# Optimization experiments

Hardware: AMD Instinct MI355X
Metric: run time of the kernel (lower is better)

## Reference

```python
import jax, jax.numpy as jnp
import numpy as np

B, L, D_MODEL = 2, 2048, 1024
HEADS, DH, K = 8, 128, 64  # d_head = d_model // heads, kernel_width window
DILATIONS = np.array([1, 1, 2, 2, 4, 4, 8, 8], dtype=np.int32)  # per-head dilation


def setup_inputs() -> dict:
    key = jax.random.key(0)
    ks = jax.random.split(key, 8)
    s_in = 1.0 / np.sqrt(D_MODEL)       # kaiming-uniform-ish fan_in bound
    s_c = 1.0 / np.sqrt(HEADS * DH)
    return {
        "query": jax.random.normal(ks[0], (B, L, D_MODEL), dtype=jnp.float32),
        "key": jax.random.normal(ks[1], (B, L, D_MODEL), dtype=jnp.float32),
        "value": jax.random.normal(ks[2], (B, L, D_MODEL), dtype=jnp.float32),
        "Wq": jax.random.uniform(ks[3], (HEADS, DH, D_MODEL), minval=-s_in, maxval=s_in),
        "bq": jnp.zeros((HEADS, DH), dtype=jnp.float32),
        "Wk": jax.random.uniform(ks[4], (HEADS, DH, D_MODEL), minval=-s_in, maxval=s_in),
        "bk": jnp.zeros((HEADS, DH), dtype=jnp.float32),
        "Wv": jax.random.uniform(ks[5], (HEADS, DH, D_MODEL), minval=-s_in, maxval=s_in),
        "bv": jnp.zeros((HEADS, DH), dtype=jnp.float32),
        "Wc": jax.random.uniform(ks[6], (D_MODEL, HEADS * DH), minval=-s_c, maxval=s_c),
        "bc": jnp.zeros((D_MODEL,), dtype=jnp.float32),
    }


def reference(query, key, value, Wq, bq, Wk, bk, Wv, bv, Wc, bc):
    Lq = query.shape[-2]
    # per-head linear projections: [B,L,D] x [H,DH,D] -> [B,H,L,DH]
    q = jnp.einsum('bld,hed->bhle', query, Wq) + bq[:, None, :]
    k = jnp.einsum('bld,hed->bhle', key, Wk) + bk[:, None, :]
    v = jnp.einsum('bld,hed->bhle', value, Wv) + bv[:, None, :]

    # dilated, centered local windows (per-head dilation)
    offsets = jnp.arange(K) - (K - 1) // 2                     # [K]
    dil = jnp.asarray(DILATIONS)                               # [H]
    idx = (jnp.arange(Lq)[None, :, None]
           + offsets[None, None, :] * dil[:, None, None])      # [H, L, K]
    valid = (idx >= 0) & (idx < Lq)
    idxc = jnp.clip(idx, 0, Lq - 1)

    # gather per-head windows: x [B,H,L,DH], idx [H,L,K] -> [B,H,L,K,DH]
    gather = jax.vmap(lambda xh, ih: xh[:, ih], in_axes=(1, 0), out_axes=1)
    k_win = gather(k, idxc)
    v_win = gather(v, idxc)

    # banded attention (original applies no 1/sqrt(d) scaling)
    scores = jnp.einsum('bhld,bhlkd->bhlk', q, k_win)
    scores = jnp.where(valid[None], scores, jnp.asarray(-1e9, scores.dtype))
    attn = jax.nn.softmax(scores, axis=-1)
    out = jnp.einsum('bhlk,bhlkd->bhld', attn, v_win)

    # merge heads and collapse back to d_model
    out = out.transpose(0, 2, 1, 3).reshape(out.shape[0], Lq, HEADS * DH)
    return out @ Wc.T + bc
```

## Files before the change

### kernel.cpp

```cpp
#include <hip/hip_runtime.h>
#include <hip/hip_bf16.h>
#include <stdint.h>

#define NB 2
#define LQ 2048
#define DMODEL 1024
#define NH 8
#define DH 128
#define KWIN 64

typedef __attribute__((ext_vector_type(8))) short short8;
typedef __attribute__((ext_vector_type(4))) float f32x4;

#define AS1 __attribute__((address_space(1)))
#define AS3 __attribute__((address_space(3)))

__device__ __forceinline__ ushort f2bf(float f) {
  uint u = __float_as_uint(f);
  return (ushort)((u + 0x7fffu + ((u >> 16) & 1u)) >> 16);
}

__global__ void cvt_all(const float4* __restrict__ q, const float4* __restrict__ k,
                        const float4* __restrict__ v, const float4* __restrict__ wq,
                        const float4* __restrict__ wk, const float4* __restrict__ wv,
                        const float4* __restrict__ wc, ushort4* __restrict__ dst) {
  const int n4in = (NB * LQ * DMODEL) / 4;
  const int n4w = (NH * DH * DMODEL) / 4;
  const int total = 3 * n4in + 4 * n4w;
  const int stride = gridDim.x * blockDim.x;
  for (int i = blockIdx.x * blockDim.x + threadIdx.x; i < total; i += stride) {
    const float4* src;
    int off;
    if (i < 3 * n4in) {
      const int r = i >> 20;
      off = i & (n4in - 1);
      src = (r == 0) ? q : ((r == 1) ? k : v);
    } else {
      const int j = i - 3 * n4in;
      const int r = j >> 18;
      off = j & (n4w - 1);
      src = (r == 0) ? wq : ((r == 1) ? wk : ((r == 2) ? wv : wc));
    }
    float4 x = src[off];
    dst[i] = make_ushort4(f2bf(x.x), f2bf(x.y), f2bf(x.z), f2bf(x.w));
  }
}

__global__ __launch_bounds__(512, 2) void gemm256_8p(
    const ushort* __restrict__ A0p, const ushort* __restrict__ B0p,
    const float* __restrict__ c0, ushort* __restrict__ D0,
    const ushort* __restrict__ A1p, const ushort* __restrict__ B1p,
    const float* __restrict__ c1, ushort* __restrict__ D1,
    const ushort* __restrict__ A2p, const ushort* __restrict__ B2p,
    const float* __restrict__ c2, ushort* __restrict__ D2,
    int M, int N, int Kd) {
  const int gx = gridDim.x, gy = gridDim.y;
  const int nblk = gx * gy * gridDim.z;
  const int fid = (blockIdx.z * gy + blockIdx.y) * gx + blockIdx.x;
  const int nid = (fid & 7) * (nblk >> 3) + (fid >> 3);
  const int z = nid / (gx * gy);
  const int rem = nid % (gx * gy);
  const int m0 = (rem / gx) * 256;
  const int n0 = (rem % gx) * 256;

  const ushort* A = (z == 0) ? A0p : ((z == 1) ? A1p : A2p);
  const ushort* Bt = (z == 0) ? B0p : ((z == 1) ? B1p : B2p);
  const float* bias = (z == 0) ? c0 : ((z == 1) ? c1 : c2);
  ushort* Cv = (z == 0) ? D0 : ((z == 1) ? D1 : D2);

  __shared__ ushort LDS[2][32768];

  const int tid = threadIdx.x;
  const int wave = tid >> 6, lane = tid & 63;
  const int wm = wave >> 2, wn = wave & 3;
  const int lrow = lane & 15, kgrp = lane >> 4;

  int offA[2][2], offB[2][2];
#pragma unroll
  for (int u = 0; u < 2; ++u)
#pragma unroll
    for (int j = 0; j < 2; ++j) {
      const int idx = j * 512 + tid;
      const int s = idx >> 3, c = idx & 7;
      const int cs = c ^ (s & 7);
      const int rA = ((s >> 6) << 7) | (u << 6) | (s & 63);
      const int rB = ((s >> 5) << 6) | (u << 5) | (s & 31);
      offA[u][j] = (m0 + rA) * Kd + cs * 8;
      offB[u][j] = (n0 + rB) * Kd + cs * 8;
    }

  auto STAGEA = [&](int bufb, int u, int T) {
    ushort* dst = &LDS[bufb][u * 8192];
#pragma unroll
    for (int j = 0; j < 2; ++j)
      __builtin_amdgcn_global_load_lds((const AS1 void*)(A + offA[u][j] + T * 64),
                                       (AS3 void*)(dst + (j * 512 + tid) * 8), 16, 0, 0);
  };
  auto STAGEB = [&](int bufb, int u, int T) {
    ushort* dst = &LDS[bufb][16384 + u * 8192];
#pragma unroll
    for (int j = 0; j < 2; ++j)
      __builtin_amdgcn_global_load_lds((const AS1 void*)(Bt + offB[u][j] + T * 64),
                                       (AS3 void*)(dst + (j * 512 + tid) * 8), 16, 0, 0);
  };

  const int sAb = (wm * 64 + lrow) * 64;
  const int sBb = (wn * 32 + lrow) * 64;
  int xk[2];
#pragma unroll
  for (int ks = 0; ks < 2; ++ks) xk[ks] = ((ks * 4 + kgrp) ^ (lrow & 7)) * 8;

  short8 af[4][2], bf[2][2][2];
  f32x4 acc[8][4] = {};

  auto RDA = [&](int bufb, int mh) {
#pragma unroll
    for (int mi = 0; mi < 4; ++mi)
#pragma unroll
      for (int ks = 0; ks < 2; ++ks)
        af[mi][ks] = *(const short8*)(&LDS[bufb][mh * 8192 + sAb + mi * 1024 + xk[ks]]);
  };
  auto RDB = [&](int bufb, int nh) {
#pragma unroll
    for (int ni = 0; ni < 2; ++ni)
#pragma unroll
      for (int ks = 0; ks < 2; ++ks)
        bf[nh][ni][ks] =
            *(const short8*)(&LDS[bufb][16384 + nh * 8192 + sBb + ni * 1024 + xk[ks]]);
  };
  auto MM = [&](int mh, int nh) {
    __builtin_amdgcn_s_setprio(1);
#pragma unroll
    for (int mi = 0; mi < 4; ++mi)
#pragma unroll
      for (int ni = 0; ni < 2; ++ni)
#pragma unroll
        for (int ks = 0; ks < 2; ++ks)
          acc[mh * 4 + mi][nh * 2 + ni] = __builtin_amdgcn_mfma_f32_16x16x32_bf16(
              af[mi][ks], bf[nh][ni][ks], acc[mh * 4 + mi][nh * 2 + ni], 0, 0, 0);
    __builtin_amdgcn_s_setprio(0);
  };

#define LGKM0()                                        \
  asm volatile("s_waitcnt lgkmcnt(0)" ::: "memory");   \
  __builtin_amdgcn_sched_barrier(0)
#define BAR() __builtin_amdgcn_s_barrier()

  const int NKT = Kd >> 6;
  const int NIT = NKT >> 1;

  STAGEA(0, 0, 0); STAGEB(0, 0, 0); STAGEA(0, 1, 0); STAGEB(0, 1, 0);
  STAGEA(1, 0, 1); STAGEB(1, 0, 1);
  asm volatile("s_waitcnt vmcnt(4)" ::: "memory");
  __builtin_amdgcn_sched_barrier(0);
  BAR();

  for (int i = 0; i < NIT; ++i) {
    const int ta = 2 * i, tb = ta + 1;
    const bool sA = (ta + 2) < NKT, sB = (tb + 2) < NKT;
    RDA(0, 0); RDB(0, 0);
    STAGEA(1, 1, tb);
    BAR(); LGKM0(); MM(0, 0); BAR();
    RDB(0, 1);
    STAGEB(1, 1, tb);
    BAR(); LGKM0(); MM(0, 1); BAR();
    RDA(0, 1);
    if (sA) STAGEA(0, 0, ta + 2);
    BAR(); LGKM0(); MM(1, 0); BAR();
    if (sA) STAGEB(0, 0, ta + 2);
    MM(1, 1);
    if (sA) asm volatile("s_waitcnt vmcnt(4)" ::: "memory");
    else    asm volatile("s_waitcnt vmcnt(0)" ::: "memory");
    __builtin_amdgcn_sched_barrier(0);
    BAR();
    RDA(1, 0); RDB(1, 0);
    if (sA) STAGEA(0, 1, ta + 2);
    BAR(); LGKM0(); MM(0, 0); BAR();
    RDB(1, 1);
    if (sA) STAGEB(0, 1, ta + 2);
    BAR(); LGKM0(); MM(0, 1); BAR();
    RDA(1, 1);
    if (sB) STAGEA(1, 0, tb + 2);
    BAR(); LGKM0(); MM(1, 0); BAR();
    if (sB) STAGEB(1, 0, tb + 2);
    MM(1, 1);
    if (sB) asm volatile("s_waitcnt vmcnt(4)" ::: "memory");
    else    asm volatile("s_waitcnt vmcnt(0)" ::: "memory");
    __builtin_amdgcn_sched_barrier(0);
    BAR();
  }
#undef LGKM0
#undef BAR

  const int cbase = n0 + wn * 64;
  const int rbase = m0 + wm * 128;
  float bv[4];
#pragma unroll
  for (int n = 0; n < 4; ++n) bv[n] = bias[cbase + n * 16 + lrow];
#pragma unroll
  for (int m = 0; m < 8; ++m)
#pragma unroll
    for (int n = 0; n < 4; ++n) {
      const int col = cbase + n * 16 + lrow;
#pragma unroll
      for (int j = 0; j < 4; ++j)
        Cv[(size_t)(rbase + m * 16 + kgrp * 4 + j) * N + col] = f2bf(acc[m][n][j] + bv[n]);
    }
}

__global__ __launch_bounds__(256, 4) void gemm_out3(
    const ushort* __restrict__ A, const ushort* __restrict__ Bt,
    const float* __restrict__ bias, float* __restrict__ Cv, int M, int N, int Kd) {
  const int gx = gridDim.x;
  const int nblk = gx * gridDim.y;
  const int fid = blockIdx.y * gx + blockIdx.x;
  const int nid = (fid & 7) * (nblk >> 3) + (fid >> 3);
  const int m0 = (nid / gx) * 64;
  const int n0 = (nid % gx) * 64;

  __shared__ ushort As[2][64 * 32];
  __shared__ ushort Bs[2][64 * 32];

  const int tid = threadIdx.x;
  const int wave = tid >> 6, lane = tid & 63;
  const int wmO = wave >> 1, wnO = wave & 1;
  const int lrow = lane & 15, kgrp = lane >> 4;

  const ushort* gA = A + (size_t)(m0 + (tid >> 2)) * Kd + (tid & 3) * 8;
  const ushort* gB = Bt + (size_t)(n0 + (tid >> 2)) * Kd + (tid & 3) * 8;

  auto stage = [&](int buf, int kt) {
    __builtin_amdgcn_global_load_lds((const AS1 void*)(gA + kt),
                                     (AS3 void*)(As[buf] + tid * 8), 16, 0, 0);
    __builtin_amdgcn_global_load_lds((const AS1 void*)(gB + kt),
                                     (AS3 void*)(Bs[buf] + tid * 8), 16, 0, 0);
  };

  f32x4 acc[2][2] = {};
  auto compute = [&](int buf) {
    short8 af[2], bfr[2];
#pragma unroll
    for (int mi = 0; mi < 2; ++mi)
      af[mi] = *(const short8*)(As[buf] + (wmO * 32 + mi * 16 + lrow) * 32 + kgrp * 8);
#pragma unroll
    for (int ni = 0; ni < 2; ++ni)
      bfr[ni] = *(const short8*)(Bs[buf] + (wnO * 32 + ni * 16 + lrow) * 32 + kgrp * 8);
#pragma unroll
    for (int mi = 0; mi < 2; ++mi)
#pragma unroll
      for (int ni = 0; ni < 2; ++ni)
        acc[mi][ni] = __builtin_amdgcn_mfma_f32_16x16x32_bf16(af[mi], bfr[ni], acc[mi][ni], 0, 0, 0);
  };

  const int nt = Kd >> 5;
  stage(0, 0);
  __syncthreads();
  int cur = 0;
  for (int it = 0; it < nt - 1; ++it) {
    stage(cur ^ 1, (it + 1) << 5);
    compute(cur);
    __syncthreads();
    cur ^= 1;
  }
  compute(cur);

  const int cbase = n0 + wnO * 32;
  const int rbase = m0 + wmO * 32;
  float bv[2];
#pragma unroll
  for (int ni = 0; ni < 2; ++ni) bv[ni] = bias[cbase + ni * 16 + lrow];
#pragma unroll
  for (int mi = 0; mi < 2; ++mi)
#pragma unroll
    for (int ni = 0; ni < 2; ++ni) {
      const int col = cbase + ni * 16 + lrow;
#pragma unroll
      for (int j = 0; j < 4; ++j)
        Cv[(size_t)(rbase + mi * 16 + kgrp * 4 + j) * N + col] = acc[mi][ni][j] + bv[ni];
    }
}

__global__ __launch_bounds__(128) void banded_attn_mfma(
    const ushort* __restrict__ qp, const ushort* __restrict__ kp,
    const ushort* __restrict__ vp, ushort* __restrict__ ao) {
  __shared__ ushort Qs[32 * 128];
  __shared__ ushort Ks[96 * 128];
  __shared__ ushort Vs[112 * 128];
  __shared__ ushort Ps[2][16 * 104];
  __shared__ ushort Os[2][16 * 128];

  const int tid = threadIdx.x;
  const int wv = tid >> 6;
  const int lane = tid & 63;
  const int lrow = lane & 15, kgrp = lane >> 4;

  const int blk = blockIdx.x;
  const int chunk = blk & 63;
  const int h = (blk >> 6) & 7;
  const int b = blk >> 9;
  const int sh = h >> 1;
  const int dil = 1 << sh;
  const int Ld = LQ >> sh;
  const int rres = chunk >> (6 - sh);
  const int tile = chunk & ((64 >> sh) - 1);
  const int t0 = tile << 5;
  const int p0 = t0 - 32;

  const size_t headoff = (size_t)h * DH;
  const size_t bbase = (size_t)b * LQ * (NH * DH);

  const int srow = lane >> 4;
  const int sc = lane & 15;
  for (int it = wv; it < 60; it += 2) {
    int rbase, pstart;
    const ushort* g;
    ushort* ld;
    if (it < 8) {
      rbase = it * 4; pstart = t0; g = qp; ld = Qs;
    } else if (it < 32) {
      rbase = (it - 8) * 4; pstart = p0; g = kp; ld = Ks;
    } else {
      rbase = (it - 32) * 4; pstart = p0; g = vp; ld = Vs;
    }
    int row = rbase + srow;
    int key = (row ^ (row >> 3)) & 7;
    int cs = sc ^ key;
    int t = pstart + row;
    t = t < 0 ? 0 : (t >= Ld ? Ld - 1 : t);
    int l = rres + t * dil;
    const ushort* src = g + bbase + (size_t)l * (NH * DH) + headoff + cs * 8;
    __builtin_amdgcn_global_load_lds((const AS1 void*)src,
                                     (AS3 void*)(ld + rbase * 128), 16, 0, 0);
  }
  __syncthreads();

  const int iblk = wv << 4;
  f32x4 accs[5] = {};
#pragma unroll
  for (int ks = 0; ks < 4; ++ks) {
    const int qrow = iblk + lrow;
    const int qslot = (ks * 4 + kgrp) ^ ((qrow ^ (qrow >> 3)) & 7);
    short8 qf = *(const short8*)(Qs + qrow * 128 + qslot * 8);
#pragma unroll
    for (int t = 0; t < 5; ++t) {
      const int krow = (wv + t) * 16 + lrow;
      const int kslot = (ks * 4 + kgrp) ^ ((krow ^ (krow >> 3)) & 7);
      short8 kf = *(const short8*)(Ks + krow * 128 + kslot * 8);
      accs[t] = __builtin_amdgcn_mfma_f32_16x16x32_bf16(qf, kf, accs[t], 0, 0, 0);
    }
  }

  float dens[4];
#pragma unroll
  for (int j = 0; j < 4; ++j) {
    const int i_b = iblk + kgrp * 4 + j;
    float mj = -1e30f;
#pragma unroll
    for (int t = 0; t < 5; ++t) {
      const int jj = (wv + t) * 16 + lrow;
      const int p = p0 + jj;
      const bool ok = (jj >= i_b + 1) && (jj <= i_b + 64) && (p >= 0) && (p < Ld);
      float v = ok ? accs[t][j] : -1e30f;
      accs[t][j] = v;
      mj = fmaxf(mj, v);
    }
#pragma unroll
    for (int off = 1; off < 16; off <<= 1) mj = fmaxf(mj, __shfl_xor(mj, off));
    float dj = 0.f;
#pragma unroll
    for (int t = 0; t < 5; ++t) {
      float e = __expf(accs[t][j] - mj);
      accs[t][j] = e;
      dj += e;
    }
#pragma unroll
    for (int off = 1; off < 16; off <<= 1) dj += __shfl_xor(dj, off);
    dens[j] = dj;
  }

  ushort* Pw = Ps[wv];
#pragma unroll
  for (int j = 0; j < 4; ++j) {
    const int prow = kgrp * 4 + j;
#pragma unroll
    for (int t = 0; t < 5; ++t) Pw[prow * 104 + t * 16 + lrow] = f2bf(accs[t][j]);
    Pw[prow * 104 + 80 + lrow] = 0;
  }

  f32x4 accv[8] = {};
#pragma unroll
  for (int ks = 0; ks < 3; ++ks) {
    short8 pf = *(const short8*)(Pw + lrow * 104 + ks * 32 + kgrp * 8);
#pragma unroll
    for (int dt = 0; dt < 8; ++dt) {
      short8 vf;
#pragma unroll
      for (int rr = 0; rr < 8; ++rr) {
        const int vrow = iblk + ks * 32 + kgrp * 8 + rr;
        const int d = dt * 16 + lrow;
        const int slot = (d >> 3) ^ ((vrow ^ (vrow >> 3)) & 7);
        vf[rr] = (short)Vs[vrow * 128 + slot * 8 + (d & 7)];
      }
      accv[dt] = __builtin_amdgcn_mfma_f32_16x16x32_bf16(pf, vf, accv[dt], 0, 0, 0);
    }
  }

  ushort* Ow = Os[wv];
#pragma unroll
  for (int j = 0; j < 4; ++j) {
    const float inv = 1.f / dens[j];
    const int orow = kgrp * 4 + j;
#pragma unroll
    for (int dt = 0; dt < 8; ++dt)
      Ow[orow * 128 + dt * 16 + lrow] = f2bf(accv[dt][j] * inv);
  }
#pragma unroll
  for (int pass = 0; pass < 4; ++pass) {
    const int i_loc = pass * 4 + srow;
    const int tq = t0 + iblk + i_loc;
    const int l = rres + tq * dil;
    short8 vvv = *(const short8*)(Ow + i_loc * 128 + sc * 8);
    *(short8*)(ao + bbase + (size_t)l * (NH * DH) + headoff + sc * 8) = vvv;
  }
}

extern "C" void kernel_launch(void* const* d_in, const int* in_sizes, int n_in,
                              void* d_out, int out_size, void* d_ws, size_t ws_size,
                              hipStream_t stream) {
  const float* q = (const float*)d_in[0];
  const float* k = (const float*)d_in[1];
  const float* v = (const float*)d_in[2];
  const float* Wq = (const float*)d_in[3];
  const float* bq = (const float*)d_in[4];
  const float* Wk = (const float*)d_in[5];
  const float* bk = (const float*)d_in[6];
  const float* Wv = (const float*)d_in[7];
  const float* bv = (const float*)d_in[8];
  const float* Wc = (const float*)d_in[9];
  const float* bc = (const float*)d_in[10];

  const size_t NIN = (size_t)NB * LQ * DMODEL;
  const size_t NW = (size_t)NH * DH * DMODEL;

  ushort* qin = (ushort*)d_ws;
  ushort* kin = qin + NIN;
  ushort* vin = kin + NIN;
  ushort* wqb = vin + NIN;
  ushort* wkb = wqb + NW;
  ushort* wvb = wkb + NW;
  ushort* wcb = wvb + NW;
  ushort* qp = wcb + NW;
  ushort* kp = qp + NIN;
  ushort* vp = kp + NIN;
  ushort* aob = vp + NIN;

  hipLaunchKernelGGL(cvt_all, dim3(2048), dim3(256), 0, stream,
                     (const float4*)q, (const float4*)k, (const float4*)v,
                     (const float4*)Wq, (const float4*)Wk, (const float4*)Wv,
                     (const float4*)Wc, (ushort4*)qin);

  dim3 g1(DMODEL / 256, (NB * LQ) / 256, 3);
  hipLaunchKernelGGL(gemm256_8p, g1, dim3(512), 0, stream,
                     qin, wqb, bq, qp,
                     kin, wkb, bk, kp,
                     vin, wvb, bv, vp,
                     NB * LQ, DMODEL, DMODEL);

  hipLaunchKernelGGL(banded_attn_mfma, dim3(NB * NH * 64), dim3(128), 0, stream,
                     qp, kp, vp, aob);

  dim3 g2(DMODEL / 64, (NB * LQ) / 64);
  hipLaunchKernelGGL(gemm_out3, g2, dim3(256), 0, stream,
                     aob, wcb, bc, (float*)d_out, NB * LQ, DMODEL, DMODEL);
}
```

Measured before the change: 93.16 us.

## Replace QKV projection GEMM with simpler tall 256x64 tiled kernel

Swaps the hand-scheduled 256x256 QKV projection GEMM, which used an XOR-swizzled LDS layout and a fine-grained barrier schedule, for a simpler 256x64 tile kernel. The new kernel uses 256 threads, a K-step of 32 and double-buffered direct-to-LDS loads. The aim is more blocks in flight and a simpler pipeline. In exchange it gets lower arithmetic reuse per tile, likely LDS bank conflicts from the unswizzled layout, and more synchronisation per unit of work.

```diff
diff --git a/kernel.cpp b/kernel.cpp
--- a/kernel.cpp
+++ b/kernel.cpp
@@ -46,12 +46,12 @@
   }
 }
 
-__global__ __launch_bounds__(512, 2) void gemm256_8p(
-    const ushort* __restrict__ A0p, const ushort* __restrict__ B0p,
+__global__ __launch_bounds__(256, 3) void gemm_qkv_tall(
+    const ushort* __restrict__ A0, const ushort* __restrict__ B0,
     const float* __restrict__ c0, ushort* __restrict__ D0,
-    const ushort* __restrict__ A1p, const ushort* __restrict__ B1p,
+    const ushort* __restrict__ A1, const ushort* __restrict__ B1,
     const float* __restrict__ c1, ushort* __restrict__ D1,
-    const ushort* __restrict__ A2p, const ushort* __restrict__ B2p,
+    const ushort* __restrict__ A2, const ushort* __restrict__ B2,
     const float* __restrict__ c2, ushort* __restrict__ D2,
     int M, int N, int Kd) {
   const int gx = gridDim.x, gy = gridDim.y;
@@ -61,150 +61,77 @@
   const int z = nid / (gx * gy);
   const int rem = nid % (gx * gy);
   const int m0 = (rem / gx) * 256;
-  const int n0 = (rem % gx) * 256;
-
-  const ushort* A = (z == 0) ? A0p : ((z == 1) ? A1p : A2p);
-  const ushort* Bt = (z == 0) ? B0p : ((z == 1) ? B1p : B2p);
+  const int n0 = (rem % gx) * 64;
+
+  const ushort* A = (z == 0) ? A0 : ((z == 1) ? A1 : A2);
+  const ushort* Bt = (z == 0) ? B0 : ((z == 1) ? B1 : B2);
   const float* bias = (z == 0) ? c0 : ((z == 1) ? c1 : c2);
   ushort* Cv = (z == 0) ? D0 : ((z == 1) ? D1 : D2);
 
-  __shared__ ushort LDS[2][32768];
+  __shared__ ushort As[2][256 * 32];
+  __shared__ ushort Bs[2][64 * 32];
 
   const int tid = threadIdx.x;
   const int wave = tid >> 6, lane = tid & 63;
-  const int wm = wave >> 2, wn = wave & 3;
   const int lrow = lane & 15, kgrp = lane >> 4;
 
-  int offA[2][2], offB[2][2];
-#pragma unroll
-  for (int u = 0; u < 2; ++u)
-#pragma unroll
-    for (int j = 0; j < 2; ++j) {
-      const int idx = j * 512 + tid;
-      const int s = idx >> 3, c = idx & 7;
-      const int cs = c ^ (s & 7);
-      const int rA = ((s >> 6) << 7) | (u << 6) | (s & 63);
-      const int rB = ((s >> 5) << 6) | (u << 5) | (s & 31);
-      offA[u][j] = (m0 + rA) * Kd + cs * 8;
-      offB[u][j] = (n0 + rB) * Kd + cs * 8;
-    }
-
-  auto STAGEA = [&](int bufb, int u, int T) {
-    ushort* dst = &LDS[bufb][u * 8192];
-#pragma unroll
-    for (int j = 0; j < 2; ++j)
-      __builtin_amdgcn_global_load_lds((const AS1 void*)(A + offA[u][j] + T * 64),
-                                       (AS3 void*)(dst + (j * 512 + tid) * 8), 16, 0, 0);
+  const ushort* gA[4];
+#pragma unroll
+  for (int j = 0; j < 4; ++j) {
+    const int c = j * 256 + tid;
+    gA[j] = A + (size_t)(m0 + (c >> 2)) * Kd + (c & 3) * 8;
+  }
+  const ushort* gB = Bt + (size_t)(n0 + (tid >> 2)) * Kd + (tid & 3) * 8;
+
+  auto stage = [&](int buf, int kt) {
+#pragma unroll
+    for (int j = 0; j < 4; ++j)
+      __builtin_amdgcn_global_load_lds((const AS1 void*)(gA[j] + kt),
+                                       (AS3 void*)(As[buf] + (j * 256 + tid) * 8), 16, 0, 0);
+    __builtin_amdgcn_global_load_lds((const AS1 void*)(gB + kt),
+                                     (AS3 void*)(Bs[buf] + tid * 8), 16, 0, 0);
   };
-  auto STAGEB = [&](int bufb, int u, int T) {
-    ushort* dst = &LDS[bufb][16384 + u * 8192];
-#pragma unroll
-    for (int j = 0; j < 2; ++j)
-      __builtin_amdgcn_global_load_lds((const AS1 void*)(Bt + offB[u][j] + T * 64),
-                                       (AS3 void*)(dst + (j * 512 + tid) * 8), 16, 0, 0);
+
+  f32x4 acc[4][4] = {};
+  auto compute = [&](int buf) {
+    short8 af[4], bfr[4];
+#pragma unroll
+    for (int mi = 0; mi < 4; ++mi)
+      af[mi] = *(const short8*)(As[buf] + (wave * 64 + mi * 16 + lrow) * 32 + kgrp * 8);
+#pragma unroll
+    for (int ni = 0; ni < 4; ++ni)
+      bfr[ni] = *(const short8*)(Bs[buf] + (ni * 16 + lrow) * 32 + kgrp * 8);
+#pragma unroll
+    for (int mi = 0; mi < 4; ++mi)
+#pragma unroll
+      for (int ni = 0; ni < 4; ++ni)
+        acc[mi][ni] = __builtin_amdgcn_mfma_f32_16x16x32_bf16(af[mi], bfr[ni], acc[mi][ni], 0, 0, 0);
   };
 
-  const int sAb = (wm * 64 + lrow) * 64;
-  const int sBb = (wn * 32 + lrow) * 64;
-  int xk[2];
-#pragma unroll
-  for (int ks = 0; ks < 2; ++ks) xk[ks] = ((ks * 4 + kgrp) ^ (lrow & 7)) * 8;
-
-  short8 af[4][2], bf[2][2][2];
-  f32x4 acc[8][4] = {};
-
-  auto RDA = [&](int bufb, int mh) {
-#pragma unroll
-    for (int mi = 0; mi < 4; ++mi)
-#pragma unroll
-      for (int ks = 0; ks < 2; ++ks)
-        af[mi][ks] = *(const short8*)(&LDS[bufb][mh * 8192 + sAb + mi * 1024 + xk[ks]]);
-  };
-  auto RDB = [&](int bufb, int nh) {
-#pragma unroll
-    for (int ni = 0; ni < 2; ++ni)
-#pragma unroll
-      for (int ks = 0; ks < 2; ++ks)
-        bf[nh][ni][ks] =
-            *(const short8*)(&LDS[bufb][16384 + nh * 8192 + sBb + ni * 1024 + xk[ks]]);
-  };
-  auto MM = [&](int mh, int nh) {
-    __builtin_amdgcn_s_setprio(1);
-#pragma unroll
-    for (int mi = 0; mi < 4; ++mi)
-#pragma unroll
-      for (int ni = 0; ni < 2; ++ni)
-#pragma unroll
-        for (int ks = 0; ks < 2; ++ks)
-          acc[mh * 4 + mi][nh * 2 + ni] = __builtin_amdgcn_mfma_f32_16x16x32_bf16(
-              af[mi][ks], bf[nh][ni][ks], acc[mh * 4 + mi][nh * 2 + ni], 0, 0, 0);
-    __builtin_amdgcn_s_setprio(0);
-  };
-
-#define LGKM0()                                        \
-  asm volatile("s_waitcnt lgkmcnt(0)" ::: "memory");   \
-  __builtin_amdgcn_sched_barrier(0)
-#define BAR() __builtin_amdgcn_s_barrier()
-
-  const int NKT = Kd >> 6;
-  const int NIT = NKT >> 1;
-
-  STAGEA(0, 0, 0); STAGEB(0, 0, 0); STAGEA(0, 1, 0); STAGEB(0, 1, 0);
-  STAGEA(1, 0, 1); STAGEB(1, 0, 1);
-  asm volatile("s_waitcnt vmcnt(4)" ::: "memory");
-  __builtin_amdgcn_sched_barrier(0);
-  BAR();
-
-  for (int i = 0; i < NIT; ++i) {
-    const int ta = 2 * i, tb = ta + 1;
-    const bool sA = (ta + 2) < NKT, sB = (tb + 2) < NKT;
-    RDA(0, 0); RDB(0, 0);
-    STAGEA(1, 1, tb);
-    BAR(); LGKM0(); MM(0, 0); BAR();
-    RDB(0, 1);
-    STAGEB(1, 1, tb);
-    BAR(); LGKM0(); MM(0, 1); BAR();
-    RDA(0, 1);
-    if (sA) STAGEA(0, 0, ta + 2);
-    BAR(); LGKM0(); MM(1, 0); BAR();
-    if (sA) STAGEB(0, 0, ta + 2);
-    MM(1, 1);
-    if (sA) asm volatile("s_waitcnt vmcnt(4)" ::: "memory");
-    else    asm volatile("s_waitcnt vmcnt(0)" ::: "memory");
-    __builtin_amdgcn_sched_barrier(0);
-    BAR();
-    RDA(1, 0); RDB(1, 0);
-    if (sA) STAGEA(0, 1, ta + 2);
-    BAR(); LGKM0(); MM(0, 0); BAR();
-    RDB(1, 1);
-    if (sA) STAGEB(0, 1, ta + 2);
-    BAR(); LGKM0(); MM(0, 1); BAR();
-    RDA(1, 1);
-    if (sB) STAGEA(1, 0, tb + 2);
-    BAR(); LGKM0(); MM(1, 0); BAR();
-    if (sB) STAGEB(1, 0, tb + 2);
-    MM(1, 1);
-    if (sB) asm volatile("s_waitcnt vmcnt(4)" ::: "memory");
-    else    asm volatile("s_waitcnt vmcnt(0)" ::: "memory");
-    __builtin_amdgcn_sched_barrier(0);
-    BAR();
-  }
-#undef LGKM0
-#undef BAR
-
-  const int cbase = n0 + wn * 64;
-  const int rbase = m0 + wm * 128;
+  const int nt = Kd >> 5;
+  stage(0, 0);
+  __syncthreads();
+  int cur = 0;
+  for (int it = 0; it < nt - 1; ++it) {
+    stage(cur ^ 1, (it + 1) << 5);
+    compute(cur);
+    __syncthreads();
+    cur ^= 1;
+  }
+  compute(cur);
+
+  const int rbase = m0 + wave * 64;
   float bv[4];
 #pragma unroll
-  for (int n = 0; n < 4; ++n) bv[n] = bias[cbase + n * 16 + lrow];
-#pragma unroll
-  for (int m = 0; m < 8; ++m)
-#pragma unroll
-    for (int n = 0; n < 4; ++n) {
-      const int col = cbase + n * 16 + lrow;
+  for (int ni = 0; ni < 4; ++ni) bv[ni] = bias[n0 + ni * 16 + lrow];
+#pragma unroll
+  for (int mi = 0; mi < 4; ++mi)
+#pragma unroll
+    for (int ni = 0; ni < 4; ++ni) {
+      const int col = n0 + ni * 16 + lrow;
 #pragma unroll
       for (int j = 0; j < 4; ++j)
-        Cv[(size_t)(rbase + m * 16 + kgrp * 4 + j) * N + col] = f2bf(acc[m][n][j] + bv[n]);
+        Cv[(size_t)(rbase + mi * 16 + kgrp * 4 + j) * N + col] = f2bf(acc[mi][ni][j] + bv[ni]);
     }
 }
 
@@ -459,8 +386,8 @@
                      (const float4*)Wq, (const float4*)Wk, (const float4*)Wv,
                      (const float4*)Wc, (ushort4*)qin);
 
-  dim3 g1(DMODEL / 256, (NB * LQ) / 256, 3);
-  hipLaunchKernelGGL(gemm256_8p, g1, dim3(512), 0, stream,
+  dim3 g1(DMODEL / 64, (NB * LQ) / 256, 3);
+  hipLaunchKernelGGL(gemm_qkv_tall, g1, dim3(256), 0, stream,
                      qin, wqb, bq, qp,
                      kin, wkb, bk, kp,
                      vin, wvb, bv, vp,
```

New measurement: 98.70 us. 6.0% more time.
